# Performance work log

Measured on AMD Instinct MI355X. Metric: run time of the kernel, lower is better.

Reference implementation:

```python
import jax, jax.numpy as jnp
import numpy as np

# pywt db4 decomposition filters (8 taps)
DEC_LO = np.array([-0.010597401784997278, 0.032883011666982945, 0.030841381835986965,
                   -0.18703481171888114, -0.02798376941698385, 0.6308807679295904,
                   0.7148465705525415, 0.23037781330885523], dtype=np.float32)
DEC_HI = np.array([-0.23037781330885523, 0.7148465705525415, -0.6308807679295904,
                   -0.02798376941698385, 0.18703481171888114, 0.030841381835986965,
                   -0.032883011666982945, -0.010597401784997278], dtype=np.float32)
LEVEL = 6
F = 8  # filter length

# pywt dwt with mode='zero' is exactly full_convolve(x, filt)[1::2].
# We realize it as a strided correlation with the flipped filters:
# out[i] = sum_j x_pad[2i+j] * filt[F-1-j], x padded left by F-2 zeros.
_KERNEL = jnp.asarray(np.stack([DEC_LO[::-1], DEC_HI[::-1]])[:, None, :])  # [2,1,F]

def _dwt_step(x):
    # x: [B, N] -> (cA [B, M], cD [B, M]) with M = floor((N+F-1)/2)
    N = x.shape[-1]
    M = (N + F - 1) // 2
    xp = jnp.pad(x, ((0, 0), (F - 2, F)))[:, None, :]          # [B,1,Npad]
    y = jax.lax.conv_general_dilated(
        xp, _KERNEL.astype(x.dtype), window_strides=(2,), padding='VALID',
        dimension_numbers=('NCH', 'OIH', 'NCH'))                # [B,2,>=M]
    return y[:, 0, :M], y[:, 1, :M]


def setup_inputs() -> dict:
    key = jax.random.key(0)
    x = jax.random.normal(key, (64, 262144), dtype=jnp.float32)
    return {"x": x}


def reference(x):
    # Cascaded 6-level db4 DWT, zero boundary mode.
    a = x
    details = []  # finest first
    for _ in range(LEVEL):
        a, d = _dwt_step(a)
        details.append(d)
    # Match torch module: details[0] = coarsest detail (pywt coeffs[1])
    return (a,) + tuple(details[::-1])
```

## Files before the change

kernel.cpp:

```cpp
#include <hip/hip_runtime.h>


#define NTHREADS 256
#define TT 64
#define LEN0 (64*TT + 378)
#define LEN1 (32*TT + 186)
#define LEN2 (16*TT + 90)
#define LEN3 (8*TT + 42)
#define LEN4 (4*TT + 18)
#define LEN5 (2*TT + 6)
#define LEN6 (TT)

#define N0 262144
#define M1 131075
#define M2 65541
#define M3 32774
#define M4 16390
#define M5 8198
#define M6 4102

#define OFF_A6 ((size_t)0)
#define OFF_D6 ((size_t)262528)
#define OFF_D5 ((size_t)525056)
#define OFF_D4 ((size_t)1049728)
#define OFF_D3 ((size_t)2098688)
#define OFF_D2 ((size_t)4196224)
#define OFF_D1 ((size_t)8390848)

__device__ __constant__ float c_lo[8] = {
    -0.010597401784997278f, 0.032883011666982945f, 0.030841381835986965f,
    -0.18703481171888114f, -0.02798376941698385f, 0.6308807679295904f,
    0.7148465705525415f, 0.23037781330885523f};
__device__ __constant__ float c_hi[8] = {
    -0.23037781330885523f, 0.7148465705525415f, -0.6308807679295904f,
    -0.02798376941698385f, 0.18703481171888114f, 0.030841381835986965f,
    -0.032883011666982945f, -0.010597401784997278f};

__device__ inline void dwt_step_lds(const float* __restrict__ s,
                                    float* __restrict__ d,
                                    int base, int len, int M, int cOff,
                                    float* __restrict__ dglob, int tid) {
  for (int l = tid; l < len; l += NTHREADS) {
    int g = base + l;
    float a = 0.f, dt = 0.f;
    if (g >= 0 && g < M) {
#pragma unroll
      for (int t = 0; t < 8; ++t) {
        float v = s[2 * l + 7 - t];
        a = fmaf(c_lo[t], v, a);
        dt = fmaf(c_hi[t], v, dt);
      }
    }
    d[l] = a;
    if (l >= cOff && g < M) dglob[g] = dt;
  }
}

__global__ __launch_bounds__(NTHREADS) void dwt6_kernel(
    const float* __restrict__ x, float* __restrict__ out) {
  const int p = blockIdx.x;
  const int row = blockIdx.y;
  const int tid = threadIdx.x;

  __shared__ float bufA[LEN0];
  __shared__ float bufB[LEN1];

  const int b6 = p * TT;
  const int b5 = 2 * b6 - 6;
  const int b4 = 2 * b5 - 6;
  const int b3 = 2 * b4 - 6;
  const int b2 = 2 * b3 - 6;
  const int b1 = 2 * b2 - 6;
  const int b0 = 2 * b1 - 6;

  const float* __restrict__ xr = x + (size_t)row * N0;
  for (int l = tid; l < LEN0; l += NTHREADS) {
    int g = b0 + l;
    bufA[l] = (g >= 0 && g < N0) ? xr[g] : 0.0f;
  }
  __syncthreads();

  dwt_step_lds(bufA, bufB, b1, LEN1, M1, 186, out + OFF_D1 + (size_t)row * M1, tid);
  __syncthreads();
  dwt_step_lds(bufB, bufA, b2, LEN2, M2, 90, out + OFF_D2 + (size_t)row * M2, tid);
  __syncthreads();
  dwt_step_lds(bufA, bufB, b3, LEN3, M3, 42, out + OFF_D3 + (size_t)row * M3, tid);
  __syncthreads();
  dwt_step_lds(bufB, bufA, b4, LEN4, M4, 18, out + OFF_D4 + (size_t)row * M4, tid);
  __syncthreads();
  dwt_step_lds(bufA, bufB, b5, LEN5, M5, 6, out + OFF_D5 + (size_t)row * M5, tid);
  __syncthreads();

  for (int l = tid; l < LEN6; l += NTHREADS) {
    int g = b6 + l;
    if (g < M6) {
      float a = 0.f, dt = 0.f;
#pragma unroll
      for (int t = 0; t < 8; ++t) {
        float v = bufB[2 * l + 7 - t];
        a = fmaf(c_lo[t], v, a);
        dt = fmaf(c_hi[t], v, dt);
      }
      out[OFF_A6 + (size_t)row * M6 + g] = a;
      out[OFF_D6 + (size_t)row * M6 + g] = dt;
    }
  }
}

extern "C" void kernel_launch(void* const* d_in, const int* in_sizes, int n_in,
                              void* d_out, int out_size, void* d_ws, size_t ws_size,
                              hipStream_t stream) {
  const float* x = (const float*)d_in[0];
  float* out = (float*)d_out;
  dim3 grid(65, 64);
  dwt6_kernel<<<grid, NTHREADS, 0, stream>>>(x, out);
}
```

Before: 137.2 us.

## Split DWT into independent level-1/2 and level-3..6 block groups with register-fused levels

Replaces the single cascaded LDS kernel with a grid of two block types. One type computes levels 1-2 details directly from input in registers. The other recomputes levels 1-2 approximations from a wider input window and then cascades levels 3-6. Loads are vectorised into even/odd-deinterleaved LDS arrays, two levels are fused per register pass, and outputs use nontemporal vector stores. This removes the many barrier-separated, poorly occupied LDS stages and the large per-block halo. In exchange it reads the input twice and does redundant recomputation in the coarse-level blocks.

```diff
diff --git a/kernel.cpp b/kernel.cpp
--- a/kernel.cpp
+++ b/kernel.cpp
@@ -1,15 +1,7 @@
 #include <hip/hip_runtime.h>
 
 
-#define NTHREADS 256
-#define TT 64
-#define LEN0 (64*TT + 378)
-#define LEN1 (32*TT + 186)
-#define LEN2 (16*TT + 90)
-#define LEN3 (8*TT + 42)
-#define LEN4 (4*TT + 18)
-#define LEN5 (2*TT + 6)
-#define LEN6 (TT)
+#define NT 128
 
 #define N0 262144
 #define M1 131075
@@ -27,91 +19,284 @@
 #define OFF_D2 ((size_t)4196224)
 #define OFF_D1 ((size_t)8390848)
 
-__device__ __constant__ float c_lo[8] = {
-    -0.010597401784997278f, 0.032883011666982945f, 0.030841381835986965f,
-    -0.18703481171888114f, -0.02798376941698385f, 0.6308807679295904f,
-    0.7148465705525415f, 0.23037781330885523f};
-__device__ __constant__ float c_hi[8] = {
-    -0.23037781330885523f, 0.7148465705525415f, -0.6308807679295904f,
-    -0.02798376941698385f, 0.18703481171888114f, 0.030841381835986965f,
-    -0.032883011666982945f, -0.010597401784997278f};
-
-__device__ inline void dwt_step_lds(const float* __restrict__ s,
-                                    float* __restrict__ d,
-                                    int base, int len, int M, int cOff,
-                                    float* __restrict__ dglob, int tid) {
-  for (int l = tid; l < len; l += NTHREADS) {
-    int g = base + l;
-    float a = 0.f, dt = 0.f;
-    if (g >= 0 && g < M) {
-#pragma unroll
-      for (int t = 0; t < 8; ++t) {
-        float v = s[2 * l + 7 - t];
-        a = fmaf(c_lo[t], v, a);
-        dt = fmaf(c_hi[t], v, dt);
-      }
-    }
-    d[l] = a;
-    if (l >= cOff && g < M) dglob[g] = dt;
+typedef float f4_t __attribute__((ext_vector_type(4)));
+typedef f4_t f4u_t __attribute__((aligned(4)));
+typedef float f2_t __attribute__((ext_vector_type(2)));
+typedef f2_t f2u_t __attribute__((aligned(4)));
+
+__device__ __constant__ float RLO[8] = {
+    0.23037781330885523f, 0.7148465705525415f, 0.6308807679295904f,
+    -0.02798376941698385f, -0.18703481171888114f, 0.030841381835986965f,
+    0.032883011666982945f, -0.010597401784997278f};
+__device__ __constant__ float RHI[8] = {
+    -0.010597401784997278f, -0.032883011666982945f, 0.030841381835986965f,
+    0.18703481171888114f, -0.02798376941698385f, -0.6308807679295904f,
+    0.7148465705525415f, -0.23037781330885523f};
+
+
+__global__ __launch_bounds__(NT, 6) void dwt_all(const float* __restrict__ x,
+                                                 float* __restrict__ out) {
+  const int bx = blockIdx.x;
+  const int row = blockIdx.y;
+  const int tid = threadIdx.x;
+  __shared__ __align__(16) float lds[3192];
+  const float* __restrict__ xr = x + (size_t)row * N0;
+
+  if (bx < 257) {
+    const int q = bx;
+    const int sb = (q << 10) - 20;
+    float2* E2 = (float2*)(lds);
+    float2* O2 = (float2*)(lds + 536);
+    for (int m = tid; m < 264; m += NT) {
+      int g = sb + 4 * m;
+      f4_t v = {0.f, 0.f, 0.f, 0.f};
+      if (g >= 0 && g <= N0 - 4) v = *(const f4_t*)(xr + g);
+      E2[m] = make_float2(v.x, v.z);
+      O2[m] = make_float2(v.y, v.w);
+    }
+    __syncthreads();
+
+    const int c = tid;
+    const f4_t* E4 = (const f4_t*)(lds);
+    const f4_t* O4 = (const f4_t*)(lds + 536);
+    f4_t ea = E4[c], eb = E4[c + 1], ec = E4[c + 2], ed = E4[c + 3];
+    f4_t oa = O4[c], ob = O4[c + 1], oc = O4[c + 2], od = O4[c + 3];
+    float e[13] = {ea.y, ea.z, ea.w, eb.x, eb.y, eb.z, eb.w,
+                   ec.x, ec.y, ec.z, ec.w, ed.x, ed.y};
+    float o[13] = {oa.y, oa.z, oa.w, ob.x, ob.y, ob.z, ob.w,
+                   oc.x, oc.y, oc.z, oc.w, od.x, od.y};
+
+    float A1[10];
+#pragma unroll
+    for (int i = 0; i < 10; ++i) {
+      float aa = 0.f;
+#pragma unroll
+      for (int t = 0; t < 4; ++t) {
+        aa = fmaf(RLO[2 * t], e[i + t], aa);
+        aa = fmaf(RLO[2 * t + 1], o[i + t], aa);
+      }
+      A1[i] = aa;
+    }
+    f4_t d1v;
+#pragma unroll
+    for (int j = 0; j < 4; ++j) {
+      float dd = 0.f;
+#pragma unroll
+      for (int t = 0; t < 4; ++t) {
+        dd = fmaf(RHI[2 * t], e[j + 6 + t], dd);
+        dd = fmaf(RHI[2 * t + 1], o[j + 6 + t], dd);
+      }
+      d1v[j] = dd;
+    }
+    float* __restrict__ gD1 = out + OFF_D1 + (size_t)row * M1;
+    const int h0 = (q << 9) + 4 * c;
+    if (h0 + 4 <= M1) {
+      __builtin_nontemporal_store(d1v, (f4u_t*)(gD1 + h0));
+    } else {
+#pragma unroll
+      for (int j = 0; j < 4; ++j)
+        if (h0 + j < M1) __builtin_nontemporal_store(d1v[j], gD1 + h0 + j);
+    }
+
+    f2_t d2v;
+#pragma unroll
+    for (int j = 0; j < 2; ++j) {
+      float dd = 0.f;
+#pragma unroll
+      for (int m = 0; m < 8; ++m) dd = fmaf(RHI[m], A1[2 * j + m], dd);
+      d2v[j] = dd;
+    }
+    float* __restrict__ gD2 = out + OFF_D2 + (size_t)row * M2;
+    const int g0 = (q << 8) + 2 * c;
+    if (g0 + 2 <= M2) {
+      __builtin_nontemporal_store(d2v, (f2u_t*)(gD2 + g0));
+    } else if (g0 < M2) {
+      __builtin_nontemporal_store(d2v[0], gD2 + g0);
+    }
+  } else {
+    const int p = bx - 257;
+    const int sb = (p << 11) - 380;
+    float2* xE2 = (float2*)(lds);
+    float2* xO2 = (float2*)(lds + 1216);
+    for (int m = tid; m < 607; m += NT) {
+      int g = sb + 4 * m;
+      f4_t v = {0.f, 0.f, 0.f, 0.f};
+      if (g >= 0 && g <= N0 - 4) v = *(const f4_t*)(xr + g);
+      xE2[m] = make_float2(v.x, v.z);
+      xO2[m] = make_float2(v.y, v.w);
+    }
+    __syncthreads();
+
+    {
+      const f4_t* E4 = (const f4_t*)(lds);
+      const f4_t* O4 = (const f4_t*)(lds + 1216);
+      float* c2E = lds + 2432;
+      float* c2O = lds + 2736;
+      for (int j = tid; j < 301; j += NT) {
+        f4_t ea = E4[j], eb = E4[j + 1], ec = E4[j + 2], ed = E4[j + 3];
+        f4_t oa = O4[j], ob = O4[j + 1], oc = O4[j + 2], od = O4[j + 3];
+        float e[13] = {ea.y, ea.z, ea.w, eb.x, eb.y, eb.z, eb.w,
+                       ec.x, ec.y, ec.z, ec.w, ed.x, ed.y};
+        float o[13] = {oa.y, oa.z, oa.w, ob.x, ob.y, ob.z, ob.w,
+                       oc.x, oc.y, oc.z, oc.w, od.x, od.y};
+        float A1[10];
+#pragma unroll
+        for (int i = 0; i < 10; ++i) {
+          float aa = 0.f;
+#pragma unroll
+          for (int t = 0; t < 4; ++t) {
+            aa = fmaf(RLO[2 * t], e[i + t], aa);
+            aa = fmaf(RLO[2 * t + 1], o[i + t], aa);
+          }
+          A1[i] = aa;
+        }
+        float a2e = 0.f, a2o = 0.f;
+#pragma unroll
+        for (int m = 0; m < 8; ++m) {
+          a2e = fmaf(RLO[m], A1[m], a2e);
+          a2o = fmaf(RLO[m], A1[m + 2], a2o);
+        }
+        c2E[j] = a2e;
+        c2O[j] = a2o;
+      }
+    }
+    __syncthreads();
+
+    if (tid < 73) {
+      const int j = tid;
+      const f4_t* E4 = (const f4_t*)(lds + 2432);
+      const f4_t* O4 = (const f4_t*)(lds + 2736);
+      f4_t ea = E4[j], eb = E4[j + 1], ec = E4[j + 2], ed = E4[j + 3];
+      f4_t oa = O4[j], ob = O4[j + 1], oc = O4[j + 2], od = O4[j + 3];
+      float e[13] = {ea.x, ea.y, ea.z, ea.w, eb.x, eb.y, eb.z,
+                     eb.w, ec.x, ec.y, ec.z, ec.w, ed.x};
+      float o[13] = {oa.x, oa.y, oa.z, oa.w, ob.x, ob.y, ob.z,
+                     ob.w, oc.x, oc.y, oc.z, oc.w, od.x};
+      float A3[10];
+#pragma unroll
+      for (int i = 0; i < 10; ++i) {
+        float aa = 0.f;
+#pragma unroll
+        for (int t = 0; t < 4; ++t) {
+          aa = fmaf(RLO[2 * t], e[i + t], aa);
+          aa = fmaf(RLO[2 * t + 1], o[i + t], aa);
+        }
+        A3[i] = aa;
+      }
+      float a4e = 0.f, a4o = 0.f;
+#pragma unroll
+      for (int m = 0; m < 8; ++m) {
+        a4e = fmaf(RLO[m], A3[m], a4e);
+        a4o = fmaf(RLO[m], A3[m + 2], a4o);
+      }
+      (lds + 3040)[j] = a4e;
+      (lds + 3116)[j] = a4o;
+
+      if (j >= 9) {
+        float d3[4];
+#pragma unroll
+        for (int s = 0; s < 4; ++s) {
+          float dd = 0.f;
+#pragma unroll
+          for (int t = 0; t < 4; ++t) {
+            dd = fmaf(RHI[2 * t], e[6 + s + t], dd);
+            dd = fmaf(RHI[2 * t + 1], o[6 + s + t], dd);
+          }
+          d3[s] = dd;
+        }
+        float* __restrict__ gD3 = out + OFF_D3 + (size_t)row * M3;
+        const int gb = (p << 8) + 4 * (j - 9);
+        if (gb + 1 < M3) {
+          f2_t v01 = {d3[0], d3[1]};
+          __builtin_nontemporal_store(v01, (f2u_t*)(gD3 + gb));
+        }
+        if (gb + 3 < M3) {
+          f2_t v23 = {d3[2], d3[3]};
+          __builtin_nontemporal_store(v23, (f2u_t*)(gD3 + gb + 2));
+        }
+        float d4e = 0.f, d4o = 0.f;
+#pragma unroll
+        for (int m = 0; m < 8; ++m) {
+          d4e = fmaf(RHI[m], A3[m], d4e);
+          d4o = fmaf(RHI[m], A3[m + 2], d4o);
+        }
+        float* __restrict__ gD4 = out + OFF_D4 + (size_t)row * M4;
+        const int g4 = (p << 7) + 2 * (j - 9);
+        if (g4 + 1 < M4) {
+          f2_t v = {d4e, d4o};
+          __builtin_nontemporal_store(v, (f2u_t*)(gD4 + g4));
+        }
+      }
+    }
+    __syncthreads();
+
+    if (tid < 16) {
+      const int j = tid;
+      const f4_t* E4 = (const f4_t*)(lds + 3040);
+      const f4_t* O4 = (const f4_t*)(lds + 3116);
+      f4_t ea = E4[j], eb = E4[j + 1], ec = E4[j + 2], ed = E4[j + 3];
+      f4_t oa = O4[j], ob = O4[j + 1], oc = O4[j + 2], od = O4[j + 3];
+      float e[13] = {ea.x, ea.y, ea.z, ea.w, eb.x, eb.y, eb.z,
+                     eb.w, ec.x, ec.y, ec.z, ec.w, ed.x};
+      float o[13] = {oa.x, oa.y, oa.z, oa.w, ob.x, ob.y, ob.z,
+                     ob.w, oc.x, oc.y, oc.z, oc.w, od.x};
+      float A5[10];
+#pragma unroll
+      for (int i = 0; i < 10; ++i) {
+        float aa = 0.f;
+#pragma unroll
+        for (int t = 0; t < 4; ++t) {
+          aa = fmaf(RLO[2 * t], e[i + t], aa);
+          aa = fmaf(RLO[2 * t + 1], o[i + t], aa);
+        }
+        A5[i] = aa;
+      }
+      float d5[4];
+#pragma unroll
+      for (int s = 0; s < 4; ++s) {
+        float dd = 0.f;
+#pragma unroll
+        for (int t = 0; t < 4; ++t) {
+          dd = fmaf(RHI[2 * t], e[6 + s + t], dd);
+          dd = fmaf(RHI[2 * t + 1], o[6 + s + t], dd);
+        }
+        d5[s] = dd;
+      }
+      float* __restrict__ gD5 = out + OFF_D5 + (size_t)row * M5;
+      const int h5 = (p << 6) + 4 * j;
+      if (h5 + 1 < M5) {
+        f2_t v01 = {d5[0], d5[1]};
+        __builtin_nontemporal_store(v01, (f2u_t*)(gD5 + h5));
+      }
+      if (h5 + 3 < M5) {
+        f2_t v23 = {d5[2], d5[3]};
+        __builtin_nontemporal_store(v23, (f2u_t*)(gD5 + h5 + 2));
+      }
+      float a6e = 0.f, a6o = 0.f, d6e = 0.f, d6o = 0.f;
+#pragma unroll
+      for (int m = 0; m < 8; ++m) {
+        a6e = fmaf(RLO[m], A5[m], a6e);
+        a6o = fmaf(RLO[m], A5[m + 2], a6o);
+        d6e = fmaf(RHI[m], A5[m], d6e);
+        d6o = fmaf(RHI[m], A5[m + 2], d6o);
+      }
+      const int g6 = (p << 5) + 2 * j;
+      if (g6 + 1 < M6) {
+        float* __restrict__ gA6 = out + OFF_A6 + (size_t)row * M6;
+        float* __restrict__ gD6 = out + OFF_D6 + (size_t)row * M6;
+        f2_t va = {a6e, a6o};
+        f2_t vd = {d6e, d6o};
+        __builtin_nontemporal_store(va, (f2u_t*)(gA6 + g6));
+        __builtin_nontemporal_store(vd, (f2u_t*)(gD6 + g6));
+      }
+    }
   }
 }
 
-__global__ __launch_bounds__(NTHREADS) void dwt6_kernel(
-    const float* __restrict__ x, float* __restrict__ out) {
-  const int p = blockIdx.x;
-  const int row = blockIdx.y;
-  const int tid = threadIdx.x;
-
-  __shared__ float bufA[LEN0];
-  __shared__ float bufB[LEN1];
-
-  const int b6 = p * TT;
-  const int b5 = 2 * b6 - 6;
-  const int b4 = 2 * b5 - 6;
-  const int b3 = 2 * b4 - 6;
-  const int b2 = 2 * b3 - 6;
-  const int b1 = 2 * b2 - 6;
-  const int b0 = 2 * b1 - 6;
-
-  const float* __restrict__ xr = x + (size_t)row * N0;
-  for (int l = tid; l < LEN0; l += NTHREADS) {
-    int g = b0 + l;
-    bufA[l] = (g >= 0 && g < N0) ? xr[g] : 0.0f;
-  }
-  __syncthreads();
-
-  dwt_step_lds(bufA, bufB, b1, LEN1, M1, 186, out + OFF_D1 + (size_t)row * M1, tid);
-  __syncthreads();
-  dwt_step_lds(bufB, bufA, b2, LEN2, M2, 90, out + OFF_D2 + (size_t)row * M2, tid);
-  __syncthreads();
-  dwt_step_lds(bufA, bufB, b3, LEN3, M3, 42, out + OFF_D3 + (size_t)row * M3, tid);
-  __syncthreads();
-  dwt_step_lds(bufB, bufA, b4, LEN4, M4, 18, out + OFF_D4 + (size_t)row * M4, tid);
-  __syncthreads();
-  dwt_step_lds(bufA, bufB, b5, LEN5, M5, 6, out + OFF_D5 + (size_t)row * M5, tid);
-  __syncthreads();
-
-  for (int l = tid; l < LEN6; l += NTHREADS) {
-    int g = b6 + l;
-    if (g < M6) {
-      float a = 0.f, dt = 0.f;
-#pragma unroll
-      for (int t = 0; t < 8; ++t) {
-        float v = bufB[2 * l + 7 - t];
-        a = fmaf(c_lo[t], v, a);
-        dt = fmaf(c_hi[t], v, dt);
-      }
-      out[OFF_A6 + (size_t)row * M6 + g] = a;
-      out[OFF_D6 + (size_t)row * M6 + g] = dt;
-    }
-  }
-}
-
 extern "C" void kernel_launch(void* const* d_in, const int* in_sizes, int n_in,
-                              void* d_out, int out_size, void* d_ws, size_t ws_size,
-                              hipStream_t stream) {
+                              void* d_out, int out_size, void* d_ws,
+                              size_t ws_size, hipStream_t stream) {
   const float* x = (const float*)d_in[0];
   float* out = (float*)d_out;
-  dim3 grid(65, 64);
-  dwt6_kernel<<<grid, NTHREADS, 0, stream>>>(x, out);
+  dwt_all<<<dim3(386, 64), NT, 0, stream>>>(x, out);
 }
```

Result: faster. 123.1 us (-10.3%).
